# Optimization experiments

Measured on AMD Instinct MI355X. Metric: run time of the kernel, lower is better.

Reference implementation:

```python
import jax, jax.numpy as jnp
import numpy as np

D_MODEL = 1024
N_HEADS = 16
HEAD_SIZE = D_MODEL // N_HEADS
D_FF = 4096
EPS = 1e-6


def _layernorm(x, g, b):
    # Faithful to source: (x + mean) / (std + eps), unbiased std (torch default)
    mean = jnp.mean(x, axis=-1, keepdims=True)
    std = jnp.std(x, axis=-1, keepdims=True, ddof=1)
    return g * ((x + mean) / (std + EPS)) + b


def setup_inputs() -> dict:
    key = jax.random.key(0)
    ks = jax.random.split(key, 12)
    s = lambda fan_in: 1.0 / np.sqrt(fan_in)
    x = jax.random.normal(ks[0], (4, 2048, D_MODEL), dtype=jnp.float32)
    Wq = jax.random.uniform(ks[1], (N_HEADS, D_MODEL, HEAD_SIZE), jnp.float32, -s(D_MODEL), s(D_MODEL))
    Wk = jax.random.uniform(ks[2], (N_HEADS, D_MODEL, HEAD_SIZE), jnp.float32, -s(D_MODEL), s(D_MODEL))
    Wv = jax.random.uniform(ks[3], (N_HEADS, D_MODEL, HEAD_SIZE), jnp.float32, -s(D_MODEL), s(D_MODEL))
    Wo = jax.random.uniform(ks[4], (D_MODEL, D_MODEL), jnp.float32, -s(D_MODEL), s(D_MODEL))
    bo = jax.random.uniform(ks[5], (D_MODEL,), jnp.float32, -s(D_MODEL), s(D_MODEL))
    W1 = jax.random.uniform(ks[6], (D_MODEL, D_FF), jnp.float32, -s(D_MODEL), s(D_MODEL))
    b1 = jax.random.uniform(ks[7], (D_FF,), jnp.float32, -s(D_MODEL), s(D_MODEL))
    W2 = jax.random.uniform(ks[8], (D_FF, D_MODEL), jnp.float32, -s(D_FF), s(D_FF))
    b2 = jax.random.uniform(ks[9], (D_MODEL,), jnp.float32, -s(D_FF), s(D_FF))
    g1 = jnp.ones((D_MODEL,), jnp.float32)
    be1 = jnp.zeros((D_MODEL,), jnp.float32)
    g2 = jnp.ones((D_MODEL,), jnp.float32)
    be2 = jnp.zeros((D_MODEL,), jnp.float32)
    return {"x": x, "Wq": Wq, "Wk": Wk, "Wv": Wv, "Wo": Wo, "bo": bo,
            "W1": W1, "b1": b1, "W2": W2, "b2": b2,
            "g1": g1, "be1": be1, "g2": g2, "be2": be2}


def reference(x, Wq, Wk, Wv, Wo, bo, W1, b1, W2, b2, g1, be1, g2, be2):
    # Multi-head attention; note: source scales by sqrt(d_model), not sqrt(head_size)
    scale = 1.0 / np.sqrt(D_MODEL)
    q = jnp.einsum('bsd,hde->bhse', x, Wq)
    k = jnp.einsum('bsd,hde->bhse', x, Wk)
    v = jnp.einsum('bsd,hde->bhse', x, Wv)
    scores = jnp.einsum('bhse,bhte->bhst', q, k) * scale
    attn = jax.nn.softmax(scores, axis=-1)
    o = jnp.einsum('bhst,bhte->bhse', attn, v)
    B, H, S, E = o.shape
    o = o.transpose(0, 2, 1, 3).reshape(B, S, H * E)  # concat heads
    mha_out = o @ Wo + bo

    h1 = _layernorm(x + mha_out, g1, be1)

    ff = jax.nn.relu(h1 @ W1 + b1) @ W2 + b2
    out = _layernorm(h1 + ff, g2, be2)
    return out
```

## Files before the change

### kernel.cpp

```cpp
#include <hip/hip_runtime.h>

typedef short short8 __attribute__((ext_vector_type(8)));
typedef short short4v __attribute__((ext_vector_type(4)));
typedef float floatx4 __attribute__((ext_vector_type(4)));

#define D_MODEL 1024
#define N_HEADS 16
#define HEAD    64
#define D_FF    4096
#define SEQ     2048
#define BATCH   4
#define TOKENS  (BATCH*SEQ)

__device__ __forceinline__ float b2f(unsigned short u) {
  return __uint_as_float(((unsigned)u) << 16);
}
__device__ __forceinline__ unsigned short f2b(float f) {
  unsigned u = __float_as_uint(f);
  unsigned r = 0x7fffu + ((u >> 16) & 1u);
  return (unsigned short)((u + r) >> 16);
}
__device__ __forceinline__ floatx4 mfma16(short8 a, short8 b, floatx4 c) {
  return __builtin_amdgcn_mfma_f32_16x16x32_bf16(a, b, c, 0, 0, 0);
}
__device__ __forceinline__ void load16_lds(const unsigned short* g, unsigned short* l) {
  __builtin_amdgcn_global_load_lds((const __attribute__((address_space(1))) void*)g,
                                   (__attribute__((address_space(3))) void*)l, 16, 0, 0);
}

__global__ __launch_bounds__(256) void conv_bf16(
    const float* __restrict__ src, unsigned short* __restrict__ dst)
{
  int idx = (blockIdx.x * 256 + threadIdx.x) * 4;
  float4 v = *(const float4*)(src + idx);
  short4v o;
  o[0] = (short)f2b(v.x); o[1] = (short)f2b(v.y);
  o[2] = (short)f2b(v.z); o[3] = (short)f2b(v.w);
  *(short4v*)(dst + idx) = o;
}

__global__ __launch_bounds__(256) void repack_qkv(
    const float* __restrict__ Wq, const float* __restrict__ Wk,
    const float* __restrict__ Wv, unsigned short* __restrict__ dst)
{
  __shared__ float t[64][65];
  int z = blockIdx.y, sel = z >> 4, h = z & 15;
  const float* W = (sel == 0) ? Wq : ((sel == 1) ? Wk : Wv);
  const float* src = W + (size_t)h * D_MODEL * HEAD;
  int rb = blockIdx.x * 64;
#pragma unroll
  for (int i = 0; i < 16; i++) {
    int idx = i * 256 + threadIdx.x;
    int lr = idx >> 6, lc = idx & 63;
    t[lr][lc] = src[(size_t)(rb + lr) * HEAD + lc];
  }
  __syncthreads();
  unsigned short* d0 = dst + (size_t)(sel * 1024 + h * 64) * D_MODEL;
#pragma unroll
  for (int i = 0; i < 16; i++) {
    int idx = i * 256 + threadIdx.x;
    int lc = idx >> 6, lr = idx & 63;
    d0[(size_t)lc * D_MODEL + rb + lr] = f2b(t[lr][lc]);
  }
}

__global__ __launch_bounds__(256) void transpose_k(
    const float* __restrict__ src, unsigned short* __restrict__ dst, int R, int C)
{
  __shared__ float t[64][65];
  int cb = blockIdx.x * 64, rb = blockIdx.y * 64;
#pragma unroll
  for (int i = 0; i < 16; i++) {
    int idx = i * 256 + threadIdx.x;
    int lr = idx >> 6, lc = idx & 63;
    t[lr][lc] = src[(size_t)(rb + lr) * C + cb + lc];
  }
  __syncthreads();
#pragma unroll
  for (int i = 0; i < 16; i++) {
    int idx = i * 256 + threadIdx.x;
    int lc = idx >> 6, lr = idx & 63;
    dst[(size_t)(cb + lc) * R + rb + lr] = f2b(t[lr][lc]);
  }
}

__global__ __launch_bounds__(256, 2) void gemm128(
    const unsigned short* __restrict__ A, const unsigned short* __restrict__ BT,
    const float* __restrict__ biasf, const float* __restrict__ residf,
    const unsigned short* __restrict__ residb, void* __restrict__ outp,
    int M, int N, int K, int epi)
{
  __shared__ unsigned short a_sh[128 * 32];
  __shared__ unsigned short b_sh[128 * 32];

  const int tid  = threadIdx.x;
  const int lane = tid & 63;
  const int wave = tid >> 6;
  const int quad = lane >> 4;
  const int l15  = lane & 15;
  const int wm   = wave & 1;
  const int wn   = wave >> 1;
  const int m0   = blockIdx.y * 128;
  const int n0   = blockIdx.x * 128;

  const int rA = tid >> 2;
  const int kc = (tid & 3) * 8;
  const unsigned short* ag0 = A  + (size_t)(m0 + rA) * K + kc;
  const unsigned short* ag1 = A  + (size_t)(m0 + rA + 64) * K + kc;
  const unsigned short* bg0 = BT + (size_t)(n0 + rA) * K + kc;
  const unsigned short* bg1 = BT + (size_t)(n0 + rA + 64) * K + kc;
  unsigned short* la0 = a_sh + wave * 512;
  unsigned short* la1 = a_sh + 2048 + wave * 512;
  unsigned short* lb0 = b_sh + wave * 512;
  unsigned short* lb1 = b_sh + 2048 + wave * 512;

  floatx4 acc[4][4] = {};

  for (int k0 = 0; k0 < K; k0 += 32) {
    __syncthreads();
    load16_lds(ag0 + k0, la0);
    load16_lds(ag1 + k0, la1);
    load16_lds(bg0 + k0, lb0);
    load16_lds(bg1 + k0, lb1);
    __syncthreads();
    short8 aF[4], bF[4];
#pragma unroll
    for (int i = 0; i < 4; i++)
      aF[i] = *(const short8*)(a_sh + (wm * 64 + i * 16 + l15) * 32 + quad * 8);
#pragma unroll
    for (int i = 0; i < 4; i++)
      bF[i] = *(const short8*)(b_sh + (wn * 64 + i * 16 + l15) * 32 + quad * 8);
#pragma unroll
    for (int mi = 0; mi < 4; mi++)
#pragma unroll
      for (int ni = 0; ni < 4; ni++)
        acc[mi][ni] = mfma16(aF[mi], bF[ni], acc[mi][ni]);
  }

#pragma unroll
  for (int mi = 0; mi < 4; mi++) {
#pragma unroll
    for (int ni = 0; ni < 4; ni++) {
      const int col = n0 + wn * 64 + ni * 16 + l15;
      const int row0 = m0 + wm * 64 + mi * 16 + quad * 4;
      if (epi == 0) {
        int sel = col >> 10;
        int cc = col & 1023;
        int h = cc >> 6, e = cc & 63;
        int b = row0 >> 11, s0 = row0 & 2047;
        if (sel < 2) {
          unsigned short* base = (unsigned short*)outp + (size_t)sel * 8388608;
#pragma unroll
          for (int r = 0; r < 4; r++) {
            float v2 = (sel == 0) ? acc[mi][ni][r] * 0.03125f : acc[mi][ni][r];
            base[((size_t)((b * N_HEADS + h) * SEQ + (s0 + r))) * HEAD + e] = f2b(v2);
          }
        } else {
          unsigned short* base = (unsigned short*)outp + (size_t)2 * 8388608;
          short4v pk;
#pragma unroll
          for (int r = 0; r < 4; r++) pk[r] = (short)f2b(acc[mi][ni][r]);
          *(short4v*)(base + ((size_t)((b * N_HEADS + h) * HEAD + e)) * SEQ + s0) = pk;
        }
      } else if (epi == 1) {
#pragma unroll
        for (int r = 0; r < 4; r++)
          ((float*)outp)[(size_t)(row0 + r) * N + col] =
              acc[mi][ni][r] + biasf[col] + residf[(size_t)(row0 + r) * N + col];
      } else if (epi == 2) {
#pragma unroll
        for (int r = 0; r < 4; r++)
          ((unsigned short*)outp)[(size_t)(row0 + r) * N + col] =
              f2b(fmaxf(acc[mi][ni][r] + biasf[col], 0.0f));
      } else {
#pragma unroll
        for (int r = 0; r < 4; r++)
          ((float*)outp)[(size_t)(row0 + r) * N + col] =
              acc[mi][ni][r] + biasf[col] + b2f(residb[(size_t)(row0 + r) * N + col]);
      }
    }
  }
}

__global__ __launch_bounds__(256) void attn_kernel(
    const unsigned short* __restrict__ q, const unsigned short* __restrict__ k,
    const unsigned short* __restrict__ vt, unsigned short* __restrict__ o)
{
  const int bh = blockIdx.y;
  const int qt = blockIdx.x;
  const int tid = threadIdx.x, lane = tid & 63, wave = tid >> 6;
  const int quad = lane >> 4, l15 = lane & 15;
  const size_t base = (size_t)bh * SEQ * HEAD;

  __shared__ unsigned short k_sh[64 * 64];
  __shared__ unsigned short vT_sh[64 * 64];
  __shared__ unsigned short p_sh[4 * 32 * 72];
  unsigned short* pw = p_sh + wave * 32 * 72;

  short8 qf[2][2];
#pragma unroll
  for (int mi = 0; mi < 2; mi++) {
    const unsigned short* qp =
        q + base + (size_t)(qt * 128 + wave * 32 + mi * 16 + l15) * HEAD;
    qf[mi][0] = *(const short8*)(qp + quad * 8);
    qf[mi][1] = *(const short8*)(qp + 32 + quad * 8);
  }

  floatx4 oacc[2][4] = {};
  float rs[2][4] = {};

  const int r8 = lane >> 3, slot = lane & 7;

  for (int kt = 0; kt < SEQ / 64; kt++) {
    __syncthreads();
#pragma unroll
    for (int i = 0; i < 2; i++) {
      int t = wave * 16 + i * 8 + r8;
      int ck = slot ^ (t & 7);
      load16_lds(k + base + (size_t)(kt * 64 + t) * HEAD + ck * 8,
                 k_sh + (wave * 16 + i * 8) * 64);
      int cv = slot ^ (t & 7);
      load16_lds(vt + base + (size_t)t * SEQ + kt * 64 + cv * 8,
                 vT_sh + (wave * 16 + i * 8) * 64);
    }
    __syncthreads();

    floatx4 sacc[2][4] = {};
#pragma unroll
    for (int ni = 0; ni < 4; ni++) {
      int t = ni * 16 + l15;
#pragma unroll
      for (int kk = 0; kk < 2; kk++) {
        int c = kk * 4 + quad;
        short8 bf = *(const short8*)(k_sh + t * 64 + ((c ^ (t & 7)) * 8));
#pragma unroll
        for (int mi = 0; mi < 2; mi++)
          sacc[mi][ni] = mfma16(qf[mi][kk], bf, sacc[mi][ni]);
      }
    }
#pragma unroll
    for (int mi = 0; mi < 2; mi++)
#pragma unroll
      for (int ni = 0; ni < 4; ni++)
#pragma unroll
        for (int r = 0; r < 4; r++) {
          float p = __expf(sacc[mi][ni][r]);
          rs[mi][r] += p;
          pw[(mi * 16 + quad * 4 + r) * 72 + ni * 16 + l15] = f2b(p);
        }
#pragma unroll
    for (int mi = 0; mi < 2; mi++) {
      short8 pf0 = *(const short8*)(pw + (mi * 16 + l15) * 72 + quad * 8);
      short8 pf1 = *(const short8*)(pw + (mi * 16 + l15) * 72 + 32 + quad * 8);
#pragma unroll
      for (int ni = 0; ni < 4; ni++) {
        int e = ni * 16 + l15;
        short8 bv0 = *(const short8*)(vT_sh + e * 64 + ((quad ^ (e & 7)) * 8));
        short8 bv1 = *(const short8*)(vT_sh + e * 64 + (((4 + quad) ^ (e & 7)) * 8));
        oacc[mi][ni] = mfma16(pf0, bv0, oacc[mi][ni]);
        oacc[mi][ni] = mfma16(pf1, bv1, oacc[mi][ni]);
      }
    }
  }

#pragma unroll
  for (int mi = 0; mi < 2; mi++)
#pragma unroll
    for (int r = 0; r < 4; r++) {
      float s = rs[mi][r];
#pragma unroll
      for (int m = 1; m < 16; m <<= 1) s += __shfl_xor(s, m, 64);
      rs[mi][r] = s;
    }

  const int b = bh >> 4, h = bh & 15;
#pragma unroll
  for (int mi = 0; mi < 2; mi++)
#pragma unroll
    for (int r = 0; r < 4; r++) {
      int s = qt * 128 + wave * 32 + mi * 16 + quad * 4 + r;
      float inv = 1.0f / rs[mi][r];
#pragma unroll
      for (int ni = 0; ni < 4; ni++)
        o[((size_t)(b * SEQ + s)) * D_MODEL + h * HEAD + ni * 16 + l15] =
            f2b(oacc[mi][ni][r] * inv);
    }
}

__global__ __launch_bounds__(256) void ln_kernel(
    const float* __restrict__ in, const float* __restrict__ g,
    const float* __restrict__ be, void* __restrict__ outp, int write_bf16)
{
  const int row = blockIdx.x;
  const int tid = threadIdx.x;
  float4 xv4 = *(const float4*)(in + (size_t)row * D_MODEL + tid * 4);
  float xv[4] = {xv4.x, xv4.y, xv4.z, xv4.w};
  float s = xv[0] + xv[1] + xv[2] + xv[3];
  float ss = xv[0] * xv[0] + xv[1] * xv[1] + xv[2] * xv[2] + xv[3] * xv[3];
#pragma unroll
  for (int m = 1; m < 64; m <<= 1) {
    s += __shfl_xor(s, m, 64);
    ss += __shfl_xor(ss, m, 64);
  }
  __shared__ float red[8];
  const int wave = tid >> 6;
  if ((tid & 63) == 0) { red[wave] = s; red[4 + wave] = ss; }
  __syncthreads();
  s = red[0] + red[1] + red[2] + red[3];
  ss = red[4] + red[5] + red[6] + red[7];
  float mean = s * (1.0f / 1024.0f);
  float var = fmaxf((ss - 1024.0f * mean * mean) * (1.0f / 1023.0f), 0.0f);
  float inv = 1.0f / (sqrtf(var) + 1e-6f);
  if (write_bf16) {
    short4v o4;
#pragma unroll
    for (int j = 0; j < 4; j++) {
      int c = tid * 4 + j;
      o4[j] = (short)f2b(g[c] * ((xv[j] + mean) * inv) + be[c]);
    }
    *(short4v*)((unsigned short*)outp + (size_t)row * D_MODEL + tid * 4) = o4;
  } else {
    float4 o4;
    float* ov = (float*)&o4;
#pragma unroll
    for (int j = 0; j < 4; j++) {
      int c = tid * 4 + j;
      ov[j] = g[c] * ((xv[j] + mean) * inv) + be[c];
    }
    *(float4*)((float*)outp + (size_t)row * D_MODEL + tid * 4) = o4;
  }
}

extern "C" void kernel_launch(void* const* d_in, const int* in_sizes, int n_in,
                              void* d_out, int out_size, void* d_ws, size_t ws_size,
                              hipStream_t stream)
{
  const float* x   = (const float*)d_in[0];
  const float* Wq  = (const float*)d_in[1];
  const float* Wk  = (const float*)d_in[2];
  const float* Wv  = (const float*)d_in[3];
  const float* Wo  = (const float*)d_in[4];
  const float* bo  = (const float*)d_in[5];
  const float* W1  = (const float*)d_in[6];
  const float* b1  = (const float*)d_in[7];
  const float* W2  = (const float*)d_in[8];
  const float* b2  = (const float*)d_in[9];
  const float* g1  = (const float*)d_in[10];
  const float* be1 = (const float*)d_in[11];
  const float* g2  = (const float*)d_in[12];
  const float* be2 = (const float*)d_in[13];
  float* out = (float*)d_out;

  unsigned short* ws     = (unsigned short*)d_ws;
  unsigned short* w1_bt  = ws;
  unsigned short* w2_bt  = ws + 4194304;
  unsigned short* qkv_bt = ws + 8388608;
  unsigned short* wo_bt  = ws + 11534336;
  unsigned short* x_bf   = ws + 12582912;
  unsigned short* qws    = ws + 20971520;
  unsigned short* kws    = ws + 29360128;
  unsigned short* vws    = ws + 37748736;
  unsigned short* ows    = x_bf;
  float*          r1     = (float*)(ws + 20971520);
  unsigned short* h1_bf  = x_bf;
  unsigned short* ff1    = ws + 20971520;

  dim3 blk(256);

  conv_bf16<<<TOKENS * D_MODEL / 1024, blk, 0, stream>>>(x, x_bf);
  repack_qkv<<<dim3(16, 48), blk, 0, stream>>>(Wq, Wk, Wv, qkv_bt);
  transpose_k<<<dim3(16, 16), blk, 0, stream>>>(Wo, wo_bt, 1024, 1024);
  transpose_k<<<dim3(64, 16), blk, 0, stream>>>(W1, w1_bt, 1024, 4096);
  transpose_k<<<dim3(16, 64), blk, 0, stream>>>(W2, w2_bt, 4096, 1024);

  gemm128<<<dim3(3072 / 128, TOKENS / 128), blk, 0, stream>>>(
      x_bf, qkv_bt, nullptr, nullptr, nullptr, qws, TOKENS, 3072, 1024, 0);
  attn_kernel<<<dim3(SEQ / 128, BATCH * N_HEADS), blk, 0, stream>>>(qws, kws, vws, ows);
  gemm128<<<dim3(1024 / 128, TOKENS / 128), blk, 0, stream>>>(
      ows, wo_bt, bo, x, nullptr, r1, TOKENS, 1024, 1024, 1);
  ln_kernel<<<TOKENS, blk, 0, stream>>>(r1, g1, be1, h1_bf, 1);
  gemm128<<<dim3(4096 / 128, TOKENS / 128), blk, 0, stream>>>(
      h1_bf, w1_bt, b1, nullptr, nullptr, ff1, TOKENS, 4096, 1024, 2);
  gemm128<<<dim3(1024 / 128, TOKENS / 128), blk, 0, stream>>>(
      ff1, w2_bt, b2, nullptr, h1_bf, out, TOKENS, 1024, 4096, 3);
  ln_kernel<<<TOKENS, blk, 0, stream>>>(out, g2, be2, out, 0);
}
```

Measured before the change: 576.4 us.

## Merge prep kernels, transpose score MFMA in attention, one-wave-per-row layernorm

Combines the input conversion and weight transposes into a single launch to remove several kernel launches. The attention loop now computes K·Q^T so each lane holds consecutive keys for one query, enabling packed 8-byte P stores to LDS and a per-lane row-sum with only two cross-quad shuffles. LayerNorm processes one row per wave, dropping the LDS reduction and barrier. P is now truncated to bf16 instead of rounded, slightly changing precision.

After: 542.6 us. 5.9% less time.

```diff
diff --git a/kernel.cpp b/kernel.cpp
--- a/kernel.cpp
+++ b/kernel.cpp
@@ -28,47 +28,11 @@
                                    (__attribute__((address_space(3))) void*)l, 16, 0, 0);
 }
 
-__global__ __launch_bounds__(256) void conv_bf16(
-    const float* __restrict__ src, unsigned short* __restrict__ dst)
-{
-  int idx = (blockIdx.x * 256 + threadIdx.x) * 4;
-  float4 v = *(const float4*)(src + idx);
-  short4v o;
-  o[0] = (short)f2b(v.x); o[1] = (short)f2b(v.y);
-  o[2] = (short)f2b(v.z); o[3] = (short)f2b(v.w);
-  *(short4v*)(dst + idx) = o;
-}
-
-__global__ __launch_bounds__(256) void repack_qkv(
-    const float* __restrict__ Wq, const float* __restrict__ Wk,
-    const float* __restrict__ Wv, unsigned short* __restrict__ dst)
-{
-  __shared__ float t[64][65];
-  int z = blockIdx.y, sel = z >> 4, h = z & 15;
-  const float* W = (sel == 0) ? Wq : ((sel == 1) ? Wk : Wv);
-  const float* src = W + (size_t)h * D_MODEL * HEAD;
-  int rb = blockIdx.x * 64;
-#pragma unroll
-  for (int i = 0; i < 16; i++) {
-    int idx = i * 256 + threadIdx.x;
-    int lr = idx >> 6, lc = idx & 63;
-    t[lr][lc] = src[(size_t)(rb + lr) * HEAD + lc];
-  }
-  __syncthreads();
-  unsigned short* d0 = dst + (size_t)(sel * 1024 + h * 64) * D_MODEL;
-#pragma unroll
-  for (int i = 0; i < 16; i++) {
-    int idx = i * 256 + threadIdx.x;
-    int lc = idx >> 6, lr = idx & 63;
-    d0[(size_t)lc * D_MODEL + rb + lr] = f2b(t[lr][lc]);
-  }
-}
-
-__global__ __launch_bounds__(256) void transpose_k(
-    const float* __restrict__ src, unsigned short* __restrict__ dst, int R, int C)
-{
-  __shared__ float t[64][65];
-  int cb = blockIdx.x * 64, rb = blockIdx.y * 64;
+__device__ __forceinline__ void transp_body(
+    const float* __restrict__ src, unsigned short* __restrict__ dst,
+    int R, int C, int bx, int by, float (*t)[65])
+{
+  int cb = bx * 64, rb = by * 64;
 #pragma unroll
   for (int i = 0; i < 16; i++) {
     int idx = i * 256 + threadIdx.x;
@@ -81,6 +45,56 @@
     int idx = i * 256 + threadIdx.x;
     int lc = idx >> 6, lr = idx & 63;
     dst[(size_t)(cb + lc) * R + rb + lr] = f2b(t[lr][lc]);
+  }
+}
+
+__global__ __launch_bounds__(256) void prep_kernel(
+    const float* __restrict__ x, unsigned short* __restrict__ x_bf,
+    const float* __restrict__ Wq, const float* __restrict__ Wk,
+    const float* __restrict__ Wv, unsigned short* __restrict__ qkv_bt,
+    const float* __restrict__ Wo, unsigned short* __restrict__ wo_bt,
+    const float* __restrict__ W1, unsigned short* __restrict__ w1_bt,
+    const float* __restrict__ W2, unsigned short* __restrict__ w2_bt)
+{
+  __shared__ float t[64][65];
+  int bid = blockIdx.x;
+  if (bid < 8192) {
+    int idx = bid * 1024 + threadIdx.x * 4;
+    float4 v = *(const float4*)(x + idx);
+    short4v o;
+    o[0] = (short)f2b(v.x); o[1] = (short)f2b(v.y);
+    o[2] = (short)f2b(v.z); o[3] = (short)f2b(v.w);
+    *(short4v*)(x_bf + idx) = o;
+  } else if (bid < 8960) {
+    int by = bid - 8192;
+    int xt = by & 15, z = by >> 4;
+    int sel = z >> 4, h = z & 15;
+    const float* W = (sel == 0) ? Wq : ((sel == 1) ? Wk : Wv);
+    const float* src = W + (size_t)h * D_MODEL * HEAD;
+    int rb = xt * 64;
+#pragma unroll
+    for (int i = 0; i < 16; i++) {
+      int idx = i * 256 + threadIdx.x;
+      int lr = idx >> 6, lc = idx & 63;
+      t[lr][lc] = src[(size_t)(rb + lr) * HEAD + lc];
+    }
+    __syncthreads();
+    unsigned short* d0 = qkv_bt + (size_t)(sel * 1024 + h * 64) * D_MODEL;
+#pragma unroll
+    for (int i = 0; i < 16; i++) {
+      int idx = i * 256 + threadIdx.x;
+      int lc = idx >> 6, lr = idx & 63;
+      d0[(size_t)lc * D_MODEL + rb + lr] = f2b(t[lr][lc]);
+    }
+  } else if (bid < 9216) {
+    int i = bid - 8960;
+    transp_body(Wo, wo_bt, 1024, 1024, i & 15, i >> 4, t);
+  } else if (bid < 10240) {
+    int i = bid - 9216;
+    transp_body(W1, w1_bt, 1024, 4096, i & 63, i >> 6, t);
+  } else {
+    int i = bid - 10240;
+    transp_body(W2, w2_bt, 4096, 1024, i & 15, i >> 4, t);
   }
 }
 
@@ -199,15 +213,15 @@
 
   short8 qf[2][2];
 #pragma unroll
-  for (int mi = 0; mi < 2; mi++) {
+  for (int mj = 0; mj < 2; mj++) {
     const unsigned short* qp =
-        q + base + (size_t)(qt * 128 + wave * 32 + mi * 16 + l15) * HEAD;
-    qf[mi][0] = *(const short8*)(qp + quad * 8);
-    qf[mi][1] = *(const short8*)(qp + 32 + quad * 8);
+        q + base + (size_t)(qt * 128 + wave * 32 + mj * 16 + l15) * HEAD;
+    qf[mj][0] = *(const short8*)(qp + quad * 8);
+    qf[mj][1] = *(const short8*)(qp + 32 + quad * 8);
   }
 
   floatx4 oacc[2][4] = {};
-  float rs[2][4] = {};
+  float rs[2] = {0.0f, 0.0f};
 
   const int r8 = lane >> 3, slot = lane & 7;
 
@@ -216,74 +230,69 @@
 #pragma unroll
     for (int i = 0; i < 2; i++) {
       int t = wave * 16 + i * 8 + r8;
-      int ck = slot ^ (t & 7);
-      load16_lds(k + base + (size_t)(kt * 64 + t) * HEAD + ck * 8,
+      int cg = slot ^ (t & 7);
+      load16_lds(k + base + (size_t)(kt * 64 + t) * HEAD + cg * 8,
                  k_sh + (wave * 16 + i * 8) * 64);
-      int cv = slot ^ (t & 7);
-      load16_lds(vt + base + (size_t)t * SEQ + kt * 64 + cv * 8,
+      load16_lds(vt + base + (size_t)t * SEQ + kt * 64 + cg * 8,
                  vT_sh + (wave * 16 + i * 8) * 64);
     }
     __syncthreads();
 
-    floatx4 sacc[2][4] = {};
-#pragma unroll
-    for (int ni = 0; ni < 4; ni++) {
-      int t = ni * 16 + l15;
-#pragma unroll
-      for (int kk = 0; kk < 2; kk++) {
-        int c = kk * 4 + quad;
-        short8 bf = *(const short8*)(k_sh + t * 64 + ((c ^ (t & 7)) * 8));
-#pragma unroll
-        for (int mi = 0; mi < 2; mi++)
-          sacc[mi][ni] = mfma16(qf[mi][kk], bf, sacc[mi][ni]);
+#pragma unroll
+    for (int ti = 0; ti < 4; ti++) {
+      int t = ti * 16 + l15;
+      short8 kf0 = *(const short8*)(k_sh + t * 64 + ((quad ^ (t & 7)) * 8));
+      short8 kf1 = *(const short8*)(k_sh + t * 64 + (((4 + quad) ^ (t & 7)) * 8));
+      floatx4 s0 = {0.f, 0.f, 0.f, 0.f}, s1 = {0.f, 0.f, 0.f, 0.f};
+      s0 = mfma16(kf0, qf[0][0], s0);
+      s0 = mfma16(kf1, qf[0][1], s0);
+      s1 = mfma16(kf0, qf[1][0], s1);
+      s1 = mfma16(kf1, qf[1][1], s1);
+#pragma unroll
+      for (int mj = 0; mj < 2; mj++) {
+        floatx4 s = mj ? s1 : s0;
+        float p0 = __expf(s[0]), p1 = __expf(s[1]);
+        float p2 = __expf(s[2]), p3 = __expf(s[3]);
+        rs[mj] += (p0 + p1) + (p2 + p3);
+        uint2 u;
+        u.x = __builtin_amdgcn_perm(__float_as_uint(p1), __float_as_uint(p0), 0x07060302u);
+        u.y = __builtin_amdgcn_perm(__float_as_uint(p3), __float_as_uint(p2), 0x07060302u);
+        *(uint2*)(pw + (mj * 16 + l15) * 72 + ti * 16 + quad * 4) = u;
       }
     }
-#pragma unroll
-    for (int mi = 0; mi < 2; mi++)
-#pragma unroll
-      for (int ni = 0; ni < 4; ni++)
-#pragma unroll
-        for (int r = 0; r < 4; r++) {
-          float p = __expf(sacc[mi][ni][r]);
-          rs[mi][r] += p;
-          pw[(mi * 16 + quad * 4 + r) * 72 + ni * 16 + l15] = f2b(p);
-        }
-#pragma unroll
-    for (int mi = 0; mi < 2; mi++) {
-      short8 pf0 = *(const short8*)(pw + (mi * 16 + l15) * 72 + quad * 8);
-      short8 pf1 = *(const short8*)(pw + (mi * 16 + l15) * 72 + 32 + quad * 8);
+
+#pragma unroll
+    for (int mj = 0; mj < 2; mj++) {
+      short8 pf0 = *(const short8*)(pw + (mj * 16 + l15) * 72 + quad * 8);
+      short8 pf1 = *(const short8*)(pw + (mj * 16 + l15) * 72 + 32 + quad * 8);
 #pragma unroll
       for (int ni = 0; ni < 4; ni++) {
         int e = ni * 16 + l15;
         short8 bv0 = *(const short8*)(vT_sh + e * 64 + ((quad ^ (e & 7)) * 8));
         short8 bv1 = *(const short8*)(vT_sh + e * 64 + (((4 + quad) ^ (e & 7)) * 8));
-        oacc[mi][ni] = mfma16(pf0, bv0, oacc[mi][ni]);
-        oacc[mi][ni] = mfma16(pf1, bv1, oacc[mi][ni]);
+        oacc[mj][ni] = mfma16(pf0, bv0, oacc[mj][ni]);
+        oacc[mj][ni] = mfma16(pf1, bv1, oacc[mj][ni]);
       }
     }
   }
 
 #pragma unroll
-  for (int mi = 0; mi < 2; mi++)
+  for (int mj = 0; mj < 2; mj++) {
+    rs[mj] += __shfl_xor(rs[mj], 16, 64);
+    rs[mj] += __shfl_xor(rs[mj], 32, 64);
+  }
+
+  const int b = bh >> 4, h = bh & 15;
+#pragma unroll
+  for (int mj = 0; mj < 2; mj++)
 #pragma unroll
     for (int r = 0; r < 4; r++) {
-      float s = rs[mi][r];
-#pragma unroll
-      for (int m = 1; m < 16; m <<= 1) s += __shfl_xor(s, m, 64);
-      rs[mi][r] = s;
-    }
-
-  const int b = bh >> 4, h = bh & 15;
-#pragma unroll
-  for (int mi = 0; mi < 2; mi++)
-#pragma unroll
-    for (int r = 0; r < 4; r++) {
-      int s = qt * 128 + wave * 32 + mi * 16 + quad * 4 + r;
-      float inv = 1.0f / rs[mi][r];
+      int s = qt * 128 + wave * 32 + mj * 16 + quad * 4 + r;
+      float inv = 1.0f / __shfl(rs[mj], quad * 4 + r, 64);
 #pragma unroll
       for (int ni = 0; ni < 4; ni++)
         o[((size_t)(b * SEQ + s)) * D_MODEL + h * HEAD + ni * 16 + l15] =
-            f2b(oacc[mi][ni][r] * inv);
+            f2b(oacc[mj][ni][r] * inv);
     }
 }
 
@@ -291,43 +300,44 @@
     const float* __restrict__ in, const float* __restrict__ g,
     const float* __restrict__ be, void* __restrict__ outp, int write_bf16)
 {
-  const int row = blockIdx.x;
-  const int tid = threadIdx.x;
-  float4 xv4 = *(const float4*)(in + (size_t)row * D_MODEL + tid * 4);
-  float xv[4] = {xv4.x, xv4.y, xv4.z, xv4.w};
-  float s = xv[0] + xv[1] + xv[2] + xv[3];
-  float ss = xv[0] * xv[0] + xv[1] * xv[1] + xv[2] * xv[2] + xv[3] * xv[3];
+  const int row = blockIdx.x * 4 + (threadIdx.x >> 6);
+  const int lane = threadIdx.x & 63;
+  const float* xp = in + (size_t)row * D_MODEL;
+  float4 xv[4];
+  float s = 0.0f, ss = 0.0f;
+#pragma unroll
+  for (int j = 0; j < 4; j++) {
+    xv[j] = *(const float4*)(xp + j * 256 + lane * 4);
+    s += (xv[j].x + xv[j].y) + (xv[j].z + xv[j].w);
+    ss += (xv[j].x * xv[j].x + xv[j].y * xv[j].y) +
+          (xv[j].z * xv[j].z + xv[j].w * xv[j].w);
+  }
 #pragma unroll
   for (int m = 1; m < 64; m <<= 1) {
     s += __shfl_xor(s, m, 64);
     ss += __shfl_xor(ss, m, 64);
   }
-  __shared__ float red[8];
-  const int wave = tid >> 6;
-  if ((tid & 63) == 0) { red[wave] = s; red[4 + wave] = ss; }
-  __syncthreads();
-  s = red[0] + red[1] + red[2] + red[3];
-  ss = red[4] + red[5] + red[6] + red[7];
   float mean = s * (1.0f / 1024.0f);
   float var = fmaxf((ss - 1024.0f * mean * mean) * (1.0f / 1023.0f), 0.0f);
   float inv = 1.0f / (sqrtf(var) + 1e-6f);
-  if (write_bf16) {
-    short4v o4;
-#pragma unroll
-    for (int j = 0; j < 4; j++) {
-      int c = tid * 4 + j;
-      o4[j] = (short)f2b(g[c] * ((xv[j] + mean) * inv) + be[c]);
-    }
-    *(short4v*)((unsigned short*)outp + (size_t)row * D_MODEL + tid * 4) = o4;
-  } else {
-    float4 o4;
-    float* ov = (float*)&o4;
-#pragma unroll
-    for (int j = 0; j < 4; j++) {
-      int c = tid * 4 + j;
-      ov[j] = g[c] * ((xv[j] + mean) * inv) + be[c];
-    }
-    *(float4*)((float*)outp + (size_t)row * D_MODEL + tid * 4) = o4;
+#pragma unroll
+  for (int j = 0; j < 4; j++) {
+    int c = j * 256 + lane * 4;
+    float4 g4 = *(const float4*)(g + c);
+    float4 b4 = *(const float4*)(be + c);
+    float y0 = g4.x * ((xv[j].x + mean) * inv) + b4.x;
+    float y1 = g4.y * ((xv[j].y + mean) * inv) + b4.y;
+    float y2 = g4.z * ((xv[j].z + mean) * inv) + b4.z;
+    float y3 = g4.w * ((xv[j].w + mean) * inv) + b4.w;
+    if (write_bf16) {
+      short4v o4;
+      o4[0] = (short)f2b(y0); o4[1] = (short)f2b(y1);
+      o4[2] = (short)f2b(y2); o4[3] = (short)f2b(y3);
+      *(short4v*)((unsigned short*)outp + (size_t)row * D_MODEL + c) = o4;
+    } else {
+      float4 o4 = {y0, y1, y2, y3};
+      *(float4*)((float*)outp + (size_t)row * D_MODEL + c) = o4;
+    }
   }
 }
 
@@ -367,21 +377,18 @@
 
   dim3 blk(256);
 
-  conv_bf16<<<TOKENS * D_MODEL / 1024, blk, 0, stream>>>(x, x_bf);
-  repack_qkv<<<dim3(16, 48), blk, 0, stream>>>(Wq, Wk, Wv, qkv_bt);
-  transpose_k<<<dim3(16, 16), blk, 0, stream>>>(Wo, wo_bt, 1024, 1024);
-  transpose_k<<<dim3(64, 16), blk, 0, stream>>>(W1, w1_bt, 1024, 4096);
-  transpose_k<<<dim3(16, 64), blk, 0, stream>>>(W2, w2_bt, 4096, 1024);
+  prep_kernel<<<11264, blk, 0, stream>>>(x, x_bf, Wq, Wk, Wv, qkv_bt,
+                                         Wo, wo_bt, W1, w1_bt, W2, w2_bt);
 
   gemm128<<<dim3(3072 / 128, TOKENS / 128), blk, 0, stream>>>(
       x_bf, qkv_bt, nullptr, nullptr, nullptr, qws, TOKENS, 3072, 1024, 0);
   attn_kernel<<<dim3(SEQ / 128, BATCH * N_HEADS), blk, 0, stream>>>(qws, kws, vws, ows);
   gemm128<<<dim3(1024 / 128, TOKENS / 128), blk, 0, stream>>>(
       ows, wo_bt, bo, x, nullptr, r1, TOKENS, 1024, 1024, 1);
-  ln_kernel<<<TOKENS, blk, 0, stream>>>(r1, g1, be1, h1_bf, 1);
+  ln_kernel<<<TOKENS / 4, blk, 0, stream>>>(r1, g1, be1, h1_bf, 1);
   gemm128<<<dim3(4096 / 128, TOKENS / 128), blk, 0, stream>>>(
       h1_bf, w1_bt, b1, nullptr, nullptr, ff1, TOKENS, 4096, 1024, 2);
   gemm128<<<dim3(1024 / 128, TOKENS / 128), blk, 0, stream>>>(
       ff1, w2_bt, b2, nullptr, h1_bf, out, TOKENS, 1024, 4096, 3);
-  ln_kernel<<<TOKENS, blk, 0, stream>>>(out, g2, be2, out, 0);
-}
+  ln_kernel<<<TOKENS / 4, blk, 0, stream>>>(out, g2, be2, out, 0);
+}
```
